# Performance work log

Hardware: AMD Instinct MI355X
Metric: run time of the kernel (lower is better)

The kernel has to match this reference:

```python
import jax, jax.numpy as jnp
import numpy as np

L, D, OC, GROUPS, EPS = 256, 1280, 128, 8, 1e-5


def setup_inputs() -> dict:
    key = jax.random.key(0)
    k1, k2 = jax.random.split(key)
    feats = jax.random.normal(k1, (L, D), dtype=jnp.float32)
    # Conv2d(3d, out_ch, kernel_size=1) weight flattened to (out_ch, 3d)
    W = jax.random.normal(k2, (OC, 3 * D), dtype=jnp.float32) * (1.0 / np.sqrt(3 * D))
    b = jnp.zeros((OC,), dtype=jnp.float32)
    gamma = jnp.ones((OC,), dtype=jnp.float32)
    beta = jnp.zeros((OC,), dtype=jnp.float32)
    return {"feats": feats, "W": W, "b": b, "gamma": gamma, "beta": beta}


def reference(feats, W, b, gamma, beta):
    fi = feats[:, None, :]                     # (L, 1, d)
    fj = feats[None, :, :]                     # (1, L, d)
    add = fi + fj                              # (L, L, d)
    diff = jnp.abs(fi - fj)                    # (L, L, d)
    had = fi * fj                              # (L, L, d)
    pair = jnp.concatenate([add, diff, had], axis=-1)  # (L, L, 3d)
    # 1x1 conv == per-pixel linear: (L, L, 3d) x (out_ch, 3d)^T -> (L, L, out_ch)
    x = jnp.einsum('ijc,oc->ijo', pair, W) + b
    # GroupNorm(8, out_ch) on batch=1: normalize over (C/g, L, L) per group
    xg = jnp.transpose(x, (2, 0, 1)).reshape(GROUPS, OC // GROUPS, L, L)
    mean = jnp.mean(xg, axis=(1, 2, 3), keepdims=True)
    var = jnp.var(xg, axis=(1, 2, 3), keepdims=True)
    xn = ((xg - mean) * jax.lax.rsqrt(var + EPS)).reshape(OC, L, L)
    xn = xn * gamma[:, None, None] + beta[:, None, None]
    out = jax.nn.gelu(xn, approximate=False)   # torch nn.GELU default = exact erf
    return out[None]                           # (1, out_ch, L, L)
```

## Files before the change

kernel.cpp:

```cpp
#include <hip/hip_runtime.h>
#include <math.h>

typedef unsigned int uint;
typedef unsigned short ushort;

typedef __attribute__((ext_vector_type(8))) __bf16 bf16x8;
typedef __attribute__((ext_vector_type(16))) float floatx16;
typedef __attribute__((ext_vector_type(2))) float f32x2;

#define NFEAT 327680
#define NW    491520

union U4B8 { uint4 u; bf16x8 b; };

__device__ inline ushort f2b(float f) {
  uint u = __float_as_uint(f);
  u += 0x7fffu + ((u >> 16) & 1u);
  return (ushort)(u >> 16);
}
__device__ inline f32x2 unpk(uint u) {
  f32x2 r;
  r.x = __uint_as_float(u << 16);
  r.y = __uint_as_float(u & 0xffff0000u);
  return r;
}

#if __has_builtin(__builtin_amdgcn_cvt_pk_bf16_f32)
typedef __attribute__((ext_vector_type(2))) __bf16 bf16x2;
__device__ inline uint cvtpk(float a, float b) {
  bf16x2 r = __builtin_amdgcn_cvt_pk_bf16_f32(a, b);
  return *(uint*)&r;
}
__device__ inline uint cvtpk_abs(float a, float b) { return cvtpk(fabsf(a), fabsf(b)); }
#else
__device__ inline uint cvtpk(float a, float b) {
  uint au = __float_as_uint(a) + 0x8000u;
  uint bu = __float_as_uint(b) + 0x8000u;
  return __builtin_amdgcn_perm(bu, au, 0x07060302u);
}
__device__ inline uint cvtpk_abs(float a, float b) { return cvtpk(a, b) & 0x7fff7fffu; }
#endif

__device__ inline void async16(const ushort* g, ushort* l) {
  __builtin_amdgcn_global_load_lds((const __attribute__((address_space(1))) uint*)g,
                                   (__attribute__((address_space(3))) uint*)l, 16, 0, 0);
}

__global__ void prep_kernel(const float* __restrict__ feats,
                            const float* __restrict__ W,
                            ushort* __restrict__ fB,
                            ushort* __restrict__ wB,
                            float* __restrict__ stats,
                            float* __restrict__ Aoi) {
  int idx = blockIdx.x * 256 + threadIdx.x;
  if (blockIdx.x == 0 && threadIdx.x < 16) stats[threadIdx.x] = 0.0f;
  if (idx < 32768) Aoi[idx] = 0.0f;
  if (idx < NFEAT) fB[idx] = f2b(feats[idx]);
  else             wB[idx - NFEAT] = f2b(W[idx - NFEAT]);
}

__global__ __launch_bounds__(256, 2) void gemma_kernel(
    const ushort* __restrict__ fB, const ushort* __restrict__ wB,
    float* __restrict__ Aoi) {
  __shared__ float red[4][1024];
  const int tid = threadIdx.x, lane = tid & 63, w = tid >> 6;
  const int i0 = (blockIdx.x >> 4) << 5;
  const int kq = (blockIdx.x >> 2) & 3;
  const int ot = blockIdx.x & 3;
  const int rr = lane & 31, half = lane >> 5;
  floatx16 a4;
  #pragma unroll
  for (int r = 0; r < 16; ++r) a4[r] = 0.0f;
  const int kbase = kq * 320 + w * 80 + half * 8;
  #pragma unroll
  for (int ks = 0; ks < 5; ++ks) {
    const int k = kbase + ks * 16;
    U4B8 bf; bf.u = *(const uint4*)(fB + (i0 + rr) * 1280 + k);
    U4B8 af; af.u = *(const uint4*)(wB + (ot * 32 + rr) * 3840 + k);
    a4 = __builtin_amdgcn_mfma_f32_32x32x16_bf16(af.b, bf.b, a4, 0, 0, 0);
  }
  #pragma unroll
  for (int r = 0; r < 16; ++r) {
    const int orow = (r & 3) + 8 * (r >> 2) + 4 * half;
    red[w][orow * 32 + rr] = a4[r];
  }
  __syncthreads();
  for (int e = tid; e < 1024; e += 256) {
    float s = red[0][e] + red[1][e] + red[2][e] + red[3][e];
    atomicAdd(&Aoi[(ot * 32 + (e >> 5)) * 256 + i0 + (e & 31)], s);
  }
}

__device__ inline void build_pair(const f32x2 jv[4], const uint4 vi, U4B8& d, U4B8& h) {
  uint iu[4] = {vi.x, vi.y, vi.z, vi.w};
  uint du[4], hu[4];
  #pragma unroll
  for (int t = 0; t < 4; ++t) {
    f32x2 fv = unpk(iu[t]);
    f32x2 dd = fv - jv[t];
    f32x2 hh = fv * jv[t];
    du[t] = cvtpk_abs(dd.x, dd.y);
    hu[t] = cvtpk(hh.x, hh.y);
  }
  d.u = make_uint4(du[0], du[1], du[2], du[3]);
  h.u = make_uint4(hu[0], hu[1], hu[2], hu[3]);
}

__global__ __launch_bounds__(256, 2) void gemm_kernel(
    const ushort* __restrict__ fB, const ushort* __restrict__ wB,
    const float* __restrict__ bias, const float* __restrict__ Aoi,
    float* __restrict__ xout, float* __restrict__ stats) {
  __shared__ __align__(16) ushort Wl[2 * 128 * 64];

  const int tid = threadIdx.x;
  const int blk = blockIdx.x;
  const int i0 = (blk >> 2) << 1;
  const int j0 = (blk & 3) << 6;
  const int lane = tid & 63;
  const int w = tid >> 6;
  const int wo = (w >> 1) << 6;
  const int wm = (w & 1) << 5;
  const int rr = lane & 31;
  const int half = lane >> 5;
  const int rr7 = lane & 7;

  const ushort* gsrc[4];
  #pragma unroll
  for (int p = 0; p < 4; ++p) {
    const int seg = w * 4 + p;
    const int row = seg * 8 + (lane >> 3);
    const int g = (lane & 7) ^ (lane >> 3);
    gsrc[p] = wB + row * 3840 + 1280 + (g >> 2) * 1280 + (g & 3) * 8;
  }

  const ushort* fi0p = fB + i0 * 1280 + half * 8;
  const ushort* fi1p = fi0p + 1280;
  const ushort* fjp = fB + (j0 + wm + rr) * 1280 + half * 8;

  floatx16 acc[2][2];
  #pragma unroll
  for (int a = 0; a < 2; ++a)
    #pragma unroll
    for (int ot = 0; ot < 2; ++ot)
      #pragma unroll
      for (int r = 0; r < 16; ++r) acc[a][ot][r] = 0.0f;

  #pragma unroll
  for (int p = 0; p < 4; ++p)
    async16(gsrc[p], &Wl[(w * 4 + p) * 512]);
  uint4 vi0[2], vi1[2], vj[2];
  #pragma unroll
  for (int st = 0; st < 2; ++st) {
    vj[st]  = *(const uint4*)(fjp  + st * 16);
    vi0[st] = *(const uint4*)(fi0p + st * 16);
    vi1[st] = *(const uint4*)(fi1p + st * 16);
  }
  __syncthreads();

  for (int cc = 0; cc < 40; ++cc) {
    const ushort* Wc = &Wl[(cc & 1) * 8192];
    uint4 vi0n[2], vi1n[2], vjn[2];
    if (cc < 39) {
      const int cn = (cc + 1) << 5;
      #pragma unroll
      for (int p = 0; p < 4; ++p)
        async16(gsrc[p] + cn, &Wl[((cc & 1) ^ 1) * 8192 + (w * 4 + p) * 512]);
      __builtin_amdgcn_sched_barrier(0);
      #pragma unroll
      for (int st = 0; st < 2; ++st) {
        vjn[st]  = *(const uint4*)(fjp  + cn + st * 16);
        vi0n[st] = *(const uint4*)(fi0p + cn + st * 16);
        vi1n[st] = *(const uint4*)(fi1p + cn + st * 16);
      }
      __builtin_amdgcn_sched_barrier(0);
    }
    #pragma unroll
    for (int st = 0; st < 2; ++st) {
      f32x2 jv[4];
      {
        uint ju[4] = {vj[st].x, vj[st].y, vj[st].z, vj[st].w};
        #pragma unroll
        for (int t = 0; t < 4; ++t) jv[t] = unpk(ju[t]);
      }
      U4B8 d0, h0, d1, h1;
      build_pair(jv, vi0[st], d0, h0);
      build_pair(jv, vi1[st], d1, h1);
      const int g0 = (st << 1) + half;
      #pragma unroll
      for (int ot = 0; ot < 2; ++ot) {
        const int rowb = (wo + ot * 32 + rr) << 6;
        bf16x8 ad = *(const bf16x8*)(Wc + rowb + ((g0 ^ rr7) << 3));
        bf16x8 ah = *(const bf16x8*)(Wc + rowb + (((g0 + 4) ^ rr7) << 3));
        acc[0][ot] = __builtin_amdgcn_mfma_f32_32x32x16_bf16(ad, d0.b, acc[0][ot], 0, 0, 0);
        acc[1][ot] = __builtin_amdgcn_mfma_f32_32x32x16_bf16(ad, d1.b, acc[1][ot], 0, 0, 0);
        acc[0][ot] = __builtin_amdgcn_mfma_f32_32x32x16_bf16(ah, h0.b, acc[0][ot], 0, 0, 0);
        acc[1][ot] = __builtin_amdgcn_mfma_f32_32x32x16_bf16(ah, h1.b, acc[1][ot], 0, 0, 0);
      }
    }
    if (cc < 39) {
      __builtin_amdgcn_sched_barrier(0);
      __builtin_amdgcn_s_waitcnt(0x0F76);
      __builtin_amdgcn_s_barrier();
      __builtin_amdgcn_sched_barrier(0);
      __asm__ volatile("" ::: "memory");
      #pragma unroll
      for (int st = 0; st < 2; ++st) {
        vj[st] = vjn[st]; vi0[st] = vi0n[st]; vi1[st] = vi1n[st];
      }
    }
  }

  float gs[2][2] = {{0.f, 0.f}, {0.f, 0.f}};
  float gq[2][2] = {{0.f, 0.f}, {0.f, 0.f}};
  const int jg = j0 + wm + rr;
  #pragma unroll
  for (int ii = 0; ii < 2; ++ii) {
    const int irow = i0 + ii;
    const int mglob = irow * 256 + jg;
    #pragma unroll
    for (int ot = 0; ot < 2; ++ot) {
      #pragma unroll
      for (int r = 0; r < 16; ++r) {
        const int orow = (r & 3) + 8 * (r >> 2) + 4 * half;
        const int o = wo + ot * 32 + orow;
        float x = acc[ii][ot][r] + Aoi[o * 256 + irow] + Aoi[o * 256 + jg] + bias[o];
        xout[o * 65536 + mglob] = x;
        gs[ot][r >> 3] += x;
        gq[ot][r >> 3] += x * x;
      }
    }
  }
  __syncthreads();
  float* sred = (float*)Wl;
  if (tid < 16) sred[tid] = 0.0f;
  __syncthreads();
  #pragma unroll
  for (int ot = 0; ot < 2; ++ot) {
    #pragma unroll
    for (int rg = 0; rg < 2; ++rg) {
      float s = gs[ot][rg], qv = gq[ot][rg];
      for (int off = 32; off > 0; off >>= 1) {
        s += __shfl_xor(s, off, 64);
        qv += __shfl_xor(qv, off, 64);
      }
      if (lane == 0) {
        const int g = (wo >> 4) + ot * 2 + rg;
        atomicAdd(&sred[g], s);
        atomicAdd(&sred[8 + g], qv);
      }
    }
  }
  __syncthreads();
  if (tid < 16) atomicAdd(&stats[tid], sred[tid]);
}

__global__ void norm_kernel(float* __restrict__ xout,
                            const float* __restrict__ stats,
                            const float* __restrict__ gamma,
                            const float* __restrict__ beta) {
  const int idx = blockIdx.x * 256 + threadIdx.x;
  const int e = idx << 2;
  const int o = e >> 16;
  const int g = o >> 4;
  const float invN = 1.0f / 1048576.0f;
  const float mean = stats[g] * invN;
  const float var = stats[8 + g] * invN - mean * mean;
  const float inv = rsqrtf(var + 1e-5f);
  const float ga = gamma[o], be = beta[o];
  float4 v = *(float4*)(xout + e);
  float* pv = &v.x;
  #pragma unroll
  for (int t = 0; t < 4; ++t) {
    float xn = (pv[t] - mean) * inv * ga + be;
    pv[t] = 0.5f * xn * (1.0f + erff(xn * 0.70710678118654752f));
  }
  *(float4*)(xout + e) = v;
}

extern "C" void kernel_launch(void* const* d_in, const int* in_sizes, int n_in,
                              void* d_out, int out_size, void* d_ws, size_t ws_size,
                              hipStream_t stream) {
  const float* feats = (const float*)d_in[0];
  const float* W     = (const float*)d_in[1];
  const float* bias  = (const float*)d_in[2];
  const float* gamma = (const float*)d_in[3];
  const float* beta  = (const float*)d_in[4];
  float* out = (float*)d_out;

  ushort* fB = (ushort*)d_ws;
  ushort* wB = fB + NFEAT;
  float* stats = (float*)(wB + NW);
  float* Aoi = stats + 16;

  prep_kernel<<<3200, 256, 0, stream>>>(feats, W, fB, wB, stats, Aoi);
  gemma_kernel<<<128, 256, 0, stream>>>(fB, wB, Aoi);
  gemm_kernel<<<512, 256, 0, stream>>>(fB, wB, bias, Aoi, out, stats);
  norm_kernel<<<8192, 256, 0, stream>>>(out, stats, gamma, beta);
}
```

Before: 154.1 us.

## Double K-chunk per iteration to halve barriers, add MFMA setprio

The main K loop now handles two 32-wide weight chunks per iteration (20 iterations instead of 40), with a 64 KB LDS double buffer holding two chunks per stage. This halves the number of workgroup barriers and waitcnt stalls. The second half's feature loads are issued inside the same iteration. s_setprio is raised around the MFMA bursts. The larger LDS footprint (64 KB per block) may lower occupancy below the two blocks per CU the launch bounds request.

```diff
diff --git a/kernel.cpp b/kernel.cpp
--- a/kernel.cpp
+++ b/kernel.cpp
@@ -110,7 +110,7 @@
     const ushort* __restrict__ fB, const ushort* __restrict__ wB,
     const float* __restrict__ bias, const float* __restrict__ Aoi,
     float* __restrict__ xout, float* __restrict__ stats) {
-  __shared__ __align__(16) ushort Wl[2 * 128 * 64];
+  __shared__ __align__(16) ushort Wl[4 * 128 * 64];
 
   const int tid = threadIdx.x;
   const int blk = blockIdx.x;
@@ -146,66 +146,90 @@
       for (int r = 0; r < 16; ++r) acc[a][ot][r] = 0.0f;
 
   #pragma unroll
-  for (int p = 0; p < 4; ++p)
-    async16(gsrc[p], &Wl[(w * 4 + p) * 512]);
+  for (int p = 0; p < 4; ++p) {
+    ushort* dst = &Wl[(w * 4 + p) * 512];
+    async16(gsrc[p], dst);
+    async16(gsrc[p] + 32, dst + 8192);
+  }
   uint4 vi0[2], vi1[2], vj[2];
   #pragma unroll
-  for (int st = 0; st < 2; ++st) {
-    vj[st]  = *(const uint4*)(fjp  + st * 16);
-    vi0[st] = *(const uint4*)(fi0p + st * 16);
-    vi1[st] = *(const uint4*)(fi1p + st * 16);
-  }
-  __syncthreads();
-
-  for (int cc = 0; cc < 40; ++cc) {
-    const ushort* Wc = &Wl[(cc & 1) * 8192];
+  for (int t = 0; t < 2; ++t) {
+    vj[t]  = *(const uint4*)(fjp  + t * 16);
+    vi0[t] = *(const uint4*)(fi0p + t * 16);
+    vi1[t] = *(const uint4*)(fi1p + t * 16);
+  }
+  __syncthreads();
+
+  for (int cc = 0; cc < 20; ++cc) {
+    const ushort* Wh = &Wl[(cc & 1) * 16384];
+    const int cb = cc << 6;
+    uint4 vj2[2], vi02[2], vi12[2];
+    #pragma unroll
+    for (int t = 0; t < 2; ++t) {
+      vj2[t]  = *(const uint4*)(fjp  + cb + (2 + t) * 16);
+      vi02[t] = *(const uint4*)(fi0p + cb + (2 + t) * 16);
+      vi12[t] = *(const uint4*)(fi1p + cb + (2 + t) * 16);
+    }
+    __builtin_amdgcn_sched_barrier(0);
     uint4 vi0n[2], vi1n[2], vjn[2];
-    if (cc < 39) {
-      const int cn = (cc + 1) << 5;
-      #pragma unroll
-      for (int p = 0; p < 4; ++p)
-        async16(gsrc[p] + cn, &Wl[((cc & 1) ^ 1) * 8192 + (w * 4 + p) * 512]);
+    if (cc < 19) {
+      const int cn = (cc + 1) << 6;
+      #pragma unroll
+      for (int p = 0; p < 4; ++p) {
+        ushort* dst = &Wl[((cc & 1) ^ 1) * 16384 + (w * 4 + p) * 512];
+        async16(gsrc[p] + cn, dst);
+        async16(gsrc[p] + cn + 32, dst + 8192);
+      }
       __builtin_amdgcn_sched_barrier(0);
       #pragma unroll
-      for (int st = 0; st < 2; ++st) {
-        vjn[st]  = *(const uint4*)(fjp  + cn + st * 16);
-        vi0n[st] = *(const uint4*)(fi0p + cn + st * 16);
-        vi1n[st] = *(const uint4*)(fi1p + cn + st * 16);
+      for (int t = 0; t < 2; ++t) {
+        vjn[t]  = *(const uint4*)(fjp  + cn + t * 16);
+        vi0n[t] = *(const uint4*)(fi0p + cn + t * 16);
+        vi1n[t] = *(const uint4*)(fi1p + cn + t * 16);
       }
       __builtin_amdgcn_sched_barrier(0);
     }
     #pragma unroll
-    for (int st = 0; st < 2; ++st) {
-      f32x2 jv[4];
-      {
-        uint ju[4] = {vj[st].x, vj[st].y, vj[st].z, vj[st].w};
+    for (int s = 0; s < 2; ++s) {
+      const ushort* Wc = Wh + s * 8192;
+      #pragma unroll
+      for (int stL = 0; stL < 2; ++stL) {
+        const uint4 vjc  = (s == 0) ? vj[stL]  : vj2[stL];
+        const uint4 vic0 = (s == 0) ? vi0[stL] : vi02[stL];
+        const uint4 vic1 = (s == 0) ? vi1[stL] : vi12[stL];
+        f32x2 jv[4];
+        {
+          uint ju[4] = {vjc.x, vjc.y, vjc.z, vjc.w};
+          #pragma unroll
+          for (int t = 0; t < 4; ++t) jv[t] = unpk(ju[t]);
+        }
+        U4B8 d0, h0, d1, h1;
+        build_pair(jv, vic0, d0, h0);
+        build_pair(jv, vic1, d1, h1);
+        const int g0 = (stL << 1) + half;
+        __builtin_amdgcn_s_setprio(1);
         #pragma unroll
-        for (int t = 0; t < 4; ++t) jv[t] = unpk(ju[t]);
-      }
-      U4B8 d0, h0, d1, h1;
-      build_pair(jv, vi0[st], d0, h0);
-      build_pair(jv, vi1[st], d1, h1);
-      const int g0 = (st << 1) + half;
-      #pragma unroll
-      for (int ot = 0; ot < 2; ++ot) {
-        const int rowb = (wo + ot * 32 + rr) << 6;
-        bf16x8 ad = *(const bf16x8*)(Wc + rowb + ((g0 ^ rr7) << 3));
-        bf16x8 ah = *(const bf16x8*)(Wc + rowb + (((g0 + 4) ^ rr7) << 3));
-        acc[0][ot] = __builtin_amdgcn_mfma_f32_32x32x16_bf16(ad, d0.b, acc[0][ot], 0, 0, 0);
-        acc[1][ot] = __builtin_amdgcn_mfma_f32_32x32x16_bf16(ad, d1.b, acc[1][ot], 0, 0, 0);
-        acc[0][ot] = __builtin_amdgcn_mfma_f32_32x32x16_bf16(ah, h0.b, acc[0][ot], 0, 0, 0);
-        acc[1][ot] = __builtin_amdgcn_mfma_f32_32x32x16_bf16(ah, h1.b, acc[1][ot], 0, 0, 0);
-      }
-    }
-    if (cc < 39) {
+        for (int ot = 0; ot < 2; ++ot) {
+          const int rowb = (wo + ot * 32 + rr) << 6;
+          bf16x8 ad = *(const bf16x8*)(Wc + rowb + ((g0 ^ rr7) << 3));
+          bf16x8 ah = *(const bf16x8*)(Wc + rowb + (((g0 + 4) ^ rr7) << 3));
+          acc[0][ot] = __builtin_amdgcn_mfma_f32_32x32x16_bf16(ad, d0.b, acc[0][ot], 0, 0, 0);
+          acc[1][ot] = __builtin_amdgcn_mfma_f32_32x32x16_bf16(ad, d1.b, acc[1][ot], 0, 0, 0);
+          acc[0][ot] = __builtin_amdgcn_mfma_f32_32x32x16_bf16(ah, h0.b, acc[0][ot], 0, 0, 0);
+          acc[1][ot] = __builtin_amdgcn_mfma_f32_32x32x16_bf16(ah, h1.b, acc[1][ot], 0, 0, 0);
+        }
+        __builtin_amdgcn_s_setprio(0);
+      }
+    }
+    if (cc < 19) {
       __builtin_amdgcn_sched_barrier(0);
       __builtin_amdgcn_s_waitcnt(0x0F76);
       __builtin_amdgcn_s_barrier();
       __builtin_amdgcn_sched_barrier(0);
       __asm__ volatile("" ::: "memory");
       #pragma unroll
-      for (int st = 0; st < 2; ++st) {
-        vj[st] = vjn[st]; vi0[st] = vi0n[st]; vi1[st] = vi1n[st];
+      for (int t = 0; t < 2; ++t) {
+        vj[t] = vjn[t]; vi0[t] = vi0n[t]; vi1[t] = vi1n[t];
       }
     }
   }
```

After: 160.5 us. 1.04x slower.
